# Performance work log

Hardware: AMD Instinct MI355X
Metric: run time of the kernel (lower is better)

Reference implementation:

```python
import jax, jax.numpy as jnp
import numpy as np

N, E, H, L, B, V = 20000, 600000, 128, 6, 16, 4


def _ln(x, g, b, eps=1e-5):
    mu = x.mean(-1, keepdims=True)
    var = ((x - mu) ** 2).mean(-1, keepdims=True)
    return (x - mu) * jax.lax.rsqrt(var + eps) * g + b


def setup_inputs() -> dict:
    key = jax.random.key(0)
    ks = jax.random.split(key, 16)
    rn = lambda k, shape, s=0.05: jax.random.normal(k, shape, jnp.float32) * s
    return dict(
        h_V=rn(ks[0], (N, H), 1.0),
        h_E=rn(ks[1], (E, H), 1.0),
        E_idx=jax.random.randint(ks[2], (2, E), 0, N, dtype=jnp.int32),
        batch_id=jnp.sort(jax.random.randint(ks[3], (N,), 0, B, dtype=jnp.int32)),
        S=jax.random.randint(ks[4], (N,), 0, V, dtype=jnp.int32),
        W1=rn(ks[5], (L, 3 * H, H)), b1=jnp.zeros((L, H), jnp.float32),
        W2=rn(ks[6], (L, H, H)), b2=jnp.zeros((L, H), jnp.float32),
        W3=rn(ks[7], (L, H, H)), b3=jnp.zeros((L, H), jnp.float32),
        ln1_g=jnp.ones((L, H), jnp.float32), ln1_b=jnp.zeros((L, H), jnp.float32),
        Wi=rn(ks[8], (L, H, 4 * H)), bi=jnp.zeros((L, 4 * H), jnp.float32),
        Wo=rn(ks[9], (L, 4 * H, H)), bo=jnp.zeros((L, H), jnp.float32),
        ln2_g=jnp.ones((L, H), jnp.float32), ln2_b=jnp.zeros((L, H), jnp.float32),
        P1=rn(ks[10], (H, H)),
        P2=rn(ks[11], (H, H)), p2b=jnp.zeros((H,), jnp.float32),
        R=rn(ks[12], (H, V)), rb=jnp.zeros((V,), jnp.float32),
    )


def reference(h_V, h_E, E_idx, batch_id, S, W1, b1, W2, b2, W3, b3,
              ln1_g, ln1_b, Wi, bi, Wo, bo, ln2_g, ln2_b, P1, P2, p2b, R, rb):
    src, dst = E_idx[0], E_idx[1]  # receiving node = src (E_idx[0])
    deg = jnp.clip(jax.ops.segment_sum(jnp.ones((E,), h_V.dtype), src,
                                       num_segments=N), 1.0)[:, None]
    for i in range(L):  # 3 encoder + 3 decoder MPNN layers, same structure
        h_EV = jnp.concatenate([h_E, h_V[src], h_V[dst]], axis=-1)  # [E, 3H]
        m = jax.nn.relu(h_EV @ W1[i] + b1[i])
        m = jax.nn.relu(m @ W2[i] + b2[i])
        m = m @ W3[i] + b3[i]
        agg = jax.ops.segment_sum(m, src, num_segments=N) / deg  # scatter_mean
        h_V = _ln(h_V + agg, ln1_g[i], ln1_b[i])
        dh = jax.nn.relu(h_V @ Wi[i] + bi[i]) @ Wo[i] + bo[i]  # position-wise FFN
        h_V = _ln(h_V + dh, ln2_g[i], ln2_b[i])
    # per-graph mean pooling (segment mean over batch_id)
    gcnt = jnp.clip(jax.ops.segment_sum(jnp.ones((N,), h_V.dtype), batch_id,
                                        num_segments=B), 1.0)[:, None]
    graph_embs = jax.ops.segment_sum(h_V, batch_id, num_segments=B) / gcnt
    graph_prjs = jax.nn.relu(graph_embs @ P1) @ P2 + p2b  # projection head
    logits = h_V @ R + rb  # readout
    return (logits, S, graph_prjs)
```

## Files before the change

kernel.cpp:

```cpp
#include <hip/hip_runtime.h>
#include <stdint.h>

#define NN 20000
#define EE 600000
#define HH 128
#define LL 6
#define BBATCH 16
#define VV 4

typedef __bf16 bf16x8 __attribute__((ext_vector_type(8)));
typedef float f32x4 __attribute__((ext_vector_type(4)));

__device__ __forceinline__ float bf2f(unsigned short u) {
    union { uint32_t i; float f; } v; v.i = ((uint32_t)u) << 16; return v.f;
}
__device__ __forceinline__ unsigned short f2bf(float f) {
    union { float f; uint32_t i; } v; v.f = f;
    uint32_t u = v.i;
    return (unsigned short)((u + 0x7FFFu + ((u >> 16) & 1u)) >> 16);
}
__device__ __forceinline__ float loadf(const void* p, size_t i, int f) {
    return f ? ((const float*)p)[i] : bf2f(((const unsigned short*)p)[i]);
}
__device__ __forceinline__ void load8bf(const void* base, size_t elem, int f, unsigned short* o) {
    if (!f) {
        *(uint4*)o = *(const uint4*)((const unsigned short*)base + elem);
    } else {
        const float* p = (const float*)base + elem;
        float4 a = *(const float4*)p, b = *(const float4*)(p + 4);
        o[0] = f2bf(a.x); o[1] = f2bf(a.y); o[2] = f2bf(a.z); o[3] = f2bf(a.w);
        o[4] = f2bf(b.x); o[5] = f2bf(b.y); o[6] = f2bf(b.z); o[7] = f2bf(b.w);
    }
}

__global__ void detect_kernel(const void* hv, int* flag) {
    __shared__ int cnt;
    if (threadIdx.x == 0) cnt = 0;
    __syncthreads();
    const unsigned short* u = (const unsigned short*)hv;
    int local = 0;
    for (int i = threadIdx.x; i < 4096; i += 256) {
        unsigned short v = u[i];
        int e = (v >> 7) & 0xFF;
        if ((v & 0x7FFF) == 0 || (e >= 0x30 && e <= 0x85)) local++;
    }
    atomicAdd(&cnt, local);
    __syncthreads();
    if (threadIdx.x == 0) flag[0] = (cnt < 3500) ? 1 : 0;
}

__global__ void repack_kernel(const void* __restrict__ src,
                              unsigned short* __restrict__ dst,
                              int K, int Nc, int total, const int* __restrict__ flag) {
    int idx = blockIdx.x * blockDim.x + threadIdx.x;
    if (idx >= total) return;
    const int f = flag[0];
    int per = K * Nc;
    int layer = idx / per, rem = idx % per;
    int k = rem / Nc, n = rem % Nc;
    dst[(size_t)layer * per + ((size_t)(k >> 5) * Nc + n) * 32 + (k & 31)] = f2bf(loadf(src, idx, f));
}

__global__ void init_hv_kernel(const void* __restrict__ hv_in,
                               float* __restrict__ hv_f32,
                               unsigned short* __restrict__ hv_bf, int total,
                               const int* __restrict__ flag) {
    int idx = blockIdx.x * blockDim.x + threadIdx.x;
    if (idx >= total) return;
    const int f = flag[0];
    float v = loadf(hv_in, idx, f);
    hv_bf[idx] = f2bf(v);
    hv_f32[idx] = v;
}

__global__ void deg_kernel(const int* __restrict__ Eidx, float* __restrict__ deg) {
    int e = blockIdx.x * blockDim.x + threadIdx.x;
    if (e < EE) atomicAdd(&deg[Eidx[e]], 1.0f);
}

__launch_bounds__(256, 3)
__global__ void edge_kernel(const void* __restrict__ hE,
                            const unsigned short* __restrict__ hv_bf,
                            const int* __restrict__ Eidx,
                            const unsigned short* __restrict__ W1p, const void* __restrict__ b1,
                            const unsigned short* __restrict__ W2p, const void* __restrict__ b2,
                            const unsigned short* __restrict__ W3p, const void* __restrict__ b3,
                            float* __restrict__ agg, int layer, const int* __restrict__ flag) {
    __shared__ __align__(16) unsigned short ev[64 * 392];
    unsigned short* m1 = ev;
    unsigned short* m2 = ev + 64 * 136;

    const int t = threadIdx.x;
    const int w = t >> 6;
    const int lane = t & 63;
    const int q = lane >> 4, ln = lane & 15;
    const int e0 = blockIdx.x * 64;
    const int f = flag[0];

    for (int c = t; c < 1024; c += 256) {
        int row = c >> 4, p = c & 15;
        int e = e0 + row;
        unsigned short tmp[8];
        load8bf(hE, (size_t)e * 128 + p * 8, f, tmp);
        *(uint4*)&ev[row * 392 + p * 8] = *(uint4*)tmp;
    }
    for (int c = t; c < 1024; c += 256) {
        int row = c >> 4, p = c & 15;
        int e = e0 + row;
        int s = Eidx[e];
        *(uint4*)&ev[row * 392 + 128 + p * 8] = *(const uint4*)&hv_bf[(size_t)s * 128 + p * 8];
    }
    for (int c = t; c < 1024; c += 256) {
        int row = c >> 4, p = c & 15;
        int e = e0 + row;
        int d = Eidx[EE + e];
        *(uint4*)&ev[row * 392 + 256 + p * 8] = *(const uint4*)&hv_bf[(size_t)d * 128 + p * 8];
    }
    __syncthreads();

    f32x4 acc[4][2];

    {
        const unsigned short* W1l = W1p + (size_t)layer * 384 * 128;
        for (int c = 0; c < 2; c++) {
            float bv = loadf(b1, (size_t)layer * HH + 16 * (2 * w + c) + ln, f);
            for (int rt = 0; rt < 4; rt++) acc[rt][c] = (f32x4){bv, bv, bv, bv};
        }
        for (int kk = 0; kk < 12; kk++) {
            bf16x8 bfr[2];
            for (int c = 0; c < 2; c++)
                bfr[c] = *(const bf16x8*)&W1l[((size_t)(kk * 128 + 16 * (2 * w + c) + ln)) * 32 + q * 8];
            for (int rt = 0; rt < 4; rt++) {
                bf16x8 af = *(bf16x8*)&ev[(16 * rt + ln) * 392 + kk * 32 + q * 8];
                acc[rt][0] = __builtin_amdgcn_mfma_f32_16x16x32_bf16(af, bfr[0], acc[rt][0], 0, 0, 0);
                acc[rt][1] = __builtin_amdgcn_mfma_f32_16x16x32_bf16(af, bfr[1], acc[rt][1], 0, 0, 0);
            }
        }
    }
    __syncthreads();
    for (int rt = 0; rt < 4; rt++)
        for (int c = 0; c < 2; c++)
            for (int r = 0; r < 4; r++) {
                float v = acc[rt][c][r]; v = v > 0.f ? v : 0.f;
                m1[(16 * rt + q * 4 + r) * 136 + 16 * (2 * w + c) + ln] = f2bf(v);
            }
    __syncthreads();

    {
        const unsigned short* W2l = W2p + (size_t)layer * 128 * 128;
        for (int c = 0; c < 2; c++) {
            float bv = loadf(b2, (size_t)layer * HH + 16 * (2 * w + c) + ln, f);
            for (int rt = 0; rt < 4; rt++) acc[rt][c] = (f32x4){bv, bv, bv, bv};
        }
        for (int kk = 0; kk < 4; kk++) {
            bf16x8 bfr[2];
            for (int c = 0; c < 2; c++)
                bfr[c] = *(const bf16x8*)&W2l[((size_t)(kk * 128 + 16 * (2 * w + c) + ln)) * 32 + q * 8];
            for (int rt = 0; rt < 4; rt++) {
                bf16x8 af = *(bf16x8*)&m1[(16 * rt + ln) * 136 + kk * 32 + q * 8];
                acc[rt][0] = __builtin_amdgcn_mfma_f32_16x16x32_bf16(af, bfr[0], acc[rt][0], 0, 0, 0);
                acc[rt][1] = __builtin_amdgcn_mfma_f32_16x16x32_bf16(af, bfr[1], acc[rt][1], 0, 0, 0);
            }
        }
    }
    for (int rt = 0; rt < 4; rt++)
        for (int c = 0; c < 2; c++)
            for (int r = 0; r < 4; r++) {
                float v = acc[rt][c][r]; v = v > 0.f ? v : 0.f;
                m2[(16 * rt + q * 4 + r) * 136 + 16 * (2 * w + c) + ln] = f2bf(v);
            }
    __syncthreads();

    {
        const unsigned short* W3l = W3p + (size_t)layer * 128 * 128;
        for (int c = 0; c < 2; c++) {
            float bv = loadf(b3, (size_t)layer * HH + 16 * (2 * w + c) + ln, f);
            for (int rt = 0; rt < 4; rt++) acc[rt][c] = (f32x4){bv, bv, bv, bv};
        }
        for (int kk = 0; kk < 4; kk++) {
            bf16x8 bfr[2];
            for (int c = 0; c < 2; c++)
                bfr[c] = *(const bf16x8*)&W3l[((size_t)(kk * 128 + 16 * (2 * w + c) + ln)) * 32 + q * 8];
            for (int rt = 0; rt < 4; rt++) {
                bf16x8 af = *(bf16x8*)&m2[(16 * rt + ln) * 136 + kk * 32 + q * 8];
                acc[rt][0] = __builtin_amdgcn_mfma_f32_16x16x32_bf16(af, bfr[0], acc[rt][0], 0, 0, 0);
                acc[rt][1] = __builtin_amdgcn_mfma_f32_16x16x32_bf16(af, bfr[1], acc[rt][1], 0, 0, 0);
            }
        }
    }

    for (int rt = 0; rt < 4; rt++) {
        int se[4];
        for (int r = 0; r < 4; r++) se[r] = Eidx[e0 + 16 * rt + q * 4 + r];
        for (int c = 0; c < 2; c++) {
            int col = 16 * (2 * w + c) + ln;
            for (int r = 0; r < 4; r++)
                atomicAdd(&agg[(size_t)se[r] * HH + col], acc[rt][c][r]);
        }
    }
}

__launch_bounds__(256, 1)
__global__ void node_kernel(float* __restrict__ hv_f32, unsigned short* __restrict__ hv_bf,
                            const float* __restrict__ agg, const float* __restrict__ deg,
                            const void* __restrict__ ln1g, const void* __restrict__ ln1b,
                            const unsigned short* __restrict__ Wip, const void* __restrict__ bip,
                            const unsigned short* __restrict__ Wop, const void* __restrict__ bop,
                            const void* __restrict__ ln2g, const void* __restrict__ ln2b,
                            int layer, const int* __restrict__ flag) {
    __shared__ __align__(16) float xf[64 * 132];
    __shared__ __align__(16) unsigned short tb[64 * 136];
    __shared__ __align__(16) unsigned short ub[64 * 520];
    const int t = threadIdx.x;
    const int w = t >> 6;
    const int lane = t & 63;
    const int q = lane >> 4, ln = lane & 15;
    const int n0 = blockIdx.x * 64;
    const int f = flag[0];

    for (int idx = t; idx < 64 * 128; idx += 256) {
        int row = idx >> 7, col = idx & 127;
        int g = n0 + row;
        float v = 0.f;
        if (g < NN) {
            float dg = deg[g]; dg = dg < 1.f ? 1.f : dg;
            v = hv_f32[(size_t)g * 128 + col] + agg[(size_t)g * 128 + col] / dg;
        }
        xf[row * 132 + col] = v;
    }
    __syncthreads();

    if (t < 64) {
        float mu = 0.f;
        for (int j = 0; j < 128; j++) mu += xf[t * 132 + j];
        mu *= (1.f / 128.f);
        float var = 0.f;
        for (int j = 0; j < 128; j++) { float d = xf[t * 132 + j] - mu; var += d * d; }
        var *= (1.f / 128.f);
        float rs = rsqrtf(var + 1e-5f);
        for (int j = 0; j < 128; j++) {
            float val = (xf[t * 132 + j] - mu) * rs * loadf(ln1g, layer * 128 + j, f)
                        + loadf(ln1b, layer * 128 + j, f);
            xf[t * 132 + j] = val;
            tb[t * 136 + j] = f2bf(val);
        }
    }
    __syncthreads();

    {
        const unsigned short* Wil = Wip + (size_t)layer * 128 * 512;
        for (int g2 = 0; g2 < 2; g2++) {
            f32x4 acc[4][4];
            for (int c = 0; c < 4; c++) {
                int ct = 8 * w + 4 * g2 + c;
                float bv = loadf(bip, (size_t)layer * 512 + 16 * ct + ln, f);
                for (int rt = 0; rt < 4; rt++) acc[rt][c] = (f32x4){bv, bv, bv, bv};
            }
            for (int kk = 0; kk < 4; kk++) {
                bf16x8 bfr[4];
                for (int c = 0; c < 4; c++) {
                    int ct = 8 * w + 4 * g2 + c;
                    bfr[c] = *(const bf16x8*)&Wil[((size_t)(kk * 512 + 16 * ct + ln)) * 32 + q * 8];
                }
                for (int rt = 0; rt < 4; rt++) {
                    bf16x8 af = *(bf16x8*)&tb[(16 * rt + ln) * 136 + kk * 32 + q * 8];
                    for (int c = 0; c < 4; c++)
                        acc[rt][c] = __builtin_amdgcn_mfma_f32_16x16x32_bf16(af, bfr[c], acc[rt][c], 0, 0, 0);
                }
            }
            for (int rt = 0; rt < 4; rt++)
                for (int c = 0; c < 4; c++) {
                    int ct = 8 * w + 4 * g2 + c;
                    for (int r = 0; r < 4; r++) {
                        float v = acc[rt][c][r]; v = v > 0.f ? v : 0.f;
                        ub[(16 * rt + q * 4 + r) * 520 + 16 * ct + ln] = f2bf(v);
                    }
                }
        }
    }
    __syncthreads();

    {
        const unsigned short* Wol = Wop + (size_t)layer * 512 * 128;
        f32x4 acc[4][2];
        for (int c = 0; c < 2; c++) {
            int ct = 2 * w + c;
            float bv = loadf(bop, (size_t)layer * 128 + 16 * ct + ln, f);
            for (int rt = 0; rt < 4; rt++) acc[rt][c] = (f32x4){bv, bv, bv, bv};
        }
        for (int kk = 0; kk < 16; kk++) {
            bf16x8 bfr[2];
            for (int c = 0; c < 2; c++) {
                int ct = 2 * w + c;
                bfr[c] = *(const bf16x8*)&Wol[((size_t)(kk * 128 + 16 * ct + ln)) * 32 + q * 8];
            }
            for (int rt = 0; rt < 4; rt++) {
                bf16x8 af = *(bf16x8*)&ub[(16 * rt + ln) * 520 + kk * 32 + q * 8];
                for (int c = 0; c < 2; c++)
                    acc[rt][c] = __builtin_amdgcn_mfma_f32_16x16x32_bf16(af, bfr[c], acc[rt][c], 0, 0, 0);
            }
        }
        for (int rt = 0; rt < 4; rt++)
            for (int c = 0; c < 2; c++) {
                int ct = 2 * w + c;
                for (int r = 0; r < 4; r++)
                    xf[(16 * rt + q * 4 + r) * 132 + 16 * ct + ln] += acc[rt][c][r];
            }
    }
    __syncthreads();

    if (t < 64) {
        int g = n0 + t;
        if (g < NN) {
            float mu = 0.f;
            for (int j = 0; j < 128; j++) mu += xf[t * 132 + j];
            mu *= (1.f / 128.f);
            float var = 0.f;
            for (int j = 0; j < 128; j++) { float d = xf[t * 132 + j] - mu; var += d * d; }
            var *= (1.f / 128.f);
            float rs = rsqrtf(var + 1e-5f);
            for (int j = 0; j < 128; j++) {
                float val = (xf[t * 132 + j] - mu) * rs * loadf(ln2g, layer * 128 + j, f)
                            + loadf(ln2b, layer * 128 + j, f);
                hv_f32[(size_t)g * 128 + j] = val;
                hv_bf[(size_t)g * 128 + j] = f2bf(val);
            }
        }
    }
}

__global__ void pool_kernel(const float* __restrict__ hv_f32, const int* __restrict__ batch_id,
                            float* __restrict__ ge) {
    int col = threadIdx.x;
    int base = blockIdx.x * 128;
    if (base >= NN) return;
    int end = base + 128; if (end > NN) end = NN;
    int cur = batch_id[base];
    float sum = 0.f;
    for (int g = base; g < end; g++) {
        int b = batch_id[g];
        if (b != cur) { atomicAdd(&ge[cur * 128 + col], sum); sum = 0.f; cur = b; }
        sum += hv_f32[(size_t)g * 128 + col];
    }
    atomicAdd(&ge[cur * 128 + col], sum);
}

__global__ void proj_kernel(const float* __restrict__ ge, const int* __restrict__ batch_id,
                            const void* __restrict__ P1, const void* __restrict__ P2,
                            const void* __restrict__ p2b, void* __restrict__ d_out,
                            const int* __restrict__ flag) {
    __shared__ float cnt[BBATCH];
    __shared__ float gm[BBATCH * HH];
    __shared__ float hb[BBATCH * HH];
    int t = threadIdx.x;
    const int f = flag[0];
    if (t < BBATCH) cnt[t] = 0.f;
    __syncthreads();
    for (int n = t; n < NN; n += 256) atomicAdd(&cnt[batch_id[n]], 1.0f);
    __syncthreads();
    for (int idx = t; idx < BBATCH * HH; idx += 256) {
        int b = idx >> 7;
        float c = cnt[b]; c = c < 1.f ? 1.f : c;
        gm[idx] = ge[idx] / c;
    }
    __syncthreads();
    for (int idx = t; idx < BBATCH * HH; idx += 256) {
        int b = idx >> 7, j = idx & 127;
        float s = 0.f;
        for (int k = 0; k < HH; k++) s += gm[b * 128 + k] * loadf(P1, k * 128 + j, f);
        hb[idx] = s > 0.f ? s : 0.f;
    }
    __syncthreads();
    for (int idx = t; idx < BBATCH * HH; idx += 256) {
        int b = idx >> 7, j = idx & 127;
        float s = loadf(p2b, j, f);
        for (int k = 0; k < HH; k++) s += hb[b * 128 + k] * loadf(P2, k * 128 + j, f);
        size_t o = (size_t)NN * VV + NN + idx;
        if (f) ((float*)d_out)[o] = s;
        else   ((unsigned short*)d_out)[o] = f2bf(s);
    }
}

__global__ void logits_kernel(const float* __restrict__ hv_f32, const void* __restrict__ R,
                              const void* __restrict__ rb, const int* __restrict__ S,
                              void* __restrict__ d_out, const int* __restrict__ flag) {
    __shared__ float Rs[HH * VV];
    __shared__ float rbs[VV];
    int t = threadIdx.x;
    const int f = flag[0];
    for (int i = t; i < HH * VV; i += 256) Rs[i] = loadf(R, i, f);
    if (t < VV) rbs[t] = loadf(rb, t, f);
    __syncthreads();
    int g = blockIdx.x * 256 + t;
    if (g < NN) {
        float a0 = rbs[0], a1 = rbs[1], a2 = rbs[2], a3 = rbs[3];
        const float* hv = hv_f32 + (size_t)g * 128;
        for (int k = 0; k < 128; k++) {
            float h = hv[k];
            a0 += h * Rs[k * 4 + 0];
            a1 += h * Rs[k * 4 + 1];
            a2 += h * Rs[k * 4 + 2];
            a3 += h * Rs[k * 4 + 3];
        }
        float sv = (float)S[g];
        if (f) {
            float* o = (float*)d_out;
            o[g * 4 + 0] = a0; o[g * 4 + 1] = a1; o[g * 4 + 2] = a2; o[g * 4 + 3] = a3;
            o[(size_t)NN * VV + g] = sv;
        } else {
            unsigned short* o = (unsigned short*)d_out;
            o[g * 4 + 0] = f2bf(a0); o[g * 4 + 1] = f2bf(a1);
            o[g * 4 + 2] = f2bf(a2); o[g * 4 + 3] = f2bf(a3);
            o[(size_t)NN * VV + g] = f2bf(sv);
        }
    }
}

extern "C" void kernel_launch(void* const* d_in, const int* in_sizes, int n_in,
                              void* d_out, int out_size, void* d_ws, size_t ws_size,
                              hipStream_t stream) {
    const void* hV   = d_in[0];
    const void* hE   = d_in[1];
    const int*  Eidx = (const int*)d_in[2];
    const int*  bid  = (const int*)d_in[3];
    const int*  S    = (const int*)d_in[4];
    const void* W1   = d_in[5];
    const void* b1   = d_in[6];
    const void* W2   = d_in[7];
    const void* b2   = d_in[8];
    const void* W3   = d_in[9];
    const void* b3   = d_in[10];
    const void* ln1g = d_in[11];
    const void* ln1b = d_in[12];
    const void* Wi   = d_in[13];
    const void* bi   = d_in[14];
    const void* Wo   = d_in[15];
    const void* bo   = d_in[16];
    const void* ln2g = d_in[17];
    const void* ln2b = d_in[18];
    const void* P1   = d_in[19];
    const void* P2   = d_in[20];
    const void* p2b  = d_in[21];
    const void* R    = d_in[22];
    const void* rb   = d_in[23];

    char* ws = (char*)d_ws;
    float* hv_f32 = (float*)ws;           ws += (size_t)NN * HH * 4;
    float* agg    = (float*)ws;           ws += (size_t)NN * HH * 4;
    float* deg    = (float*)ws;           ws += (size_t)NN * 4;
    float* ge     = (float*)ws;           ws += (size_t)BBATCH * HH * 4;
    unsigned short* hv_bf = (unsigned short*)ws; ws += (size_t)NN * HH * 2;
    unsigned short* W1p   = (unsigned short*)ws; ws += (size_t)LL * 384 * 128 * 2;
    unsigned short* W2p   = (unsigned short*)ws; ws += (size_t)LL * 128 * 128 * 2;
    unsigned short* W3p   = (unsigned short*)ws; ws += (size_t)LL * 128 * 128 * 2;
    unsigned short* Wip   = (unsigned short*)ws; ws += (size_t)LL * 128 * 512 * 2;
    unsigned short* Wop   = (unsigned short*)ws; ws += (size_t)LL * 512 * 128 * 2;
    int* flag = (int*)ws;                 ws += 16;

    hipMemsetAsync(deg, 0, (size_t)NN * 4, stream);
    hipMemsetAsync(ge, 0, (size_t)BBATCH * HH * 4, stream);

    detect_kernel<<<1, 256, 0, stream>>>(hV, flag);

    init_hv_kernel<<<(NN * HH + 255) / 256, 256, 0, stream>>>(hV, hv_f32, hv_bf, NN * HH, flag);
    deg_kernel<<<(EE + 255) / 256, 256, 0, stream>>>(Eidx, deg);

    repack_kernel<<<(LL * 384 * 128 + 255) / 256, 256, 0, stream>>>(W1, W1p, 384, 128, LL * 384 * 128, flag);
    repack_kernel<<<(LL * 128 * 128 + 255) / 256, 256, 0, stream>>>(W2, W2p, 128, 128, LL * 128 * 128, flag);
    repack_kernel<<<(LL * 128 * 128 + 255) / 256, 256, 0, stream>>>(W3, W3p, 128, 128, LL * 128 * 128, flag);
    repack_kernel<<<(LL * 128 * 512 + 255) / 256, 256, 0, stream>>>(Wi, Wip, 128, 512, LL * 128 * 512, flag);
    repack_kernel<<<(LL * 512 * 128 + 255) / 256, 256, 0, stream>>>(Wo, Wop, 512, 128, LL * 512 * 128, flag);

    for (int i = 0; i < LL; i++) {
        hipMemsetAsync(agg, 0, (size_t)NN * HH * 4, stream);
        edge_kernel<<<EE / 64, 256, 0, stream>>>(hE, hv_bf, Eidx, W1p, b1, W2p, b2, W3p, b3, agg, i, flag);
        node_kernel<<<(NN + 63) / 64, 256, 0, stream>>>(hv_f32, hv_bf, agg, deg,
                                                        ln1g, ln1b, Wip, bi, Wop, bo, ln2g, ln2b, i, flag);
    }

    pool_kernel<<<(NN + 127) / 128, 128, 0, stream>>>(hv_f32, bid, ge);
    proj_kernel<<<1, 256, 0, stream>>>(ge, bid, P1, P2, p2b, d_out, flag);
    logits_kernel<<<(NN + 255) / 256, 256, 0, stream>>>(hv_f32, R, rb, S, d_out, flag);
}
```

Baseline: 3.634 ms.

## Sort edges by source node and restructure edge MLP as per-wave 32x32 MFMA

```diff
diff --git a/kernel.cpp b/kernel.cpp
--- a/kernel.cpp
+++ b/kernel.cpp
@@ -3,6 +3,7 @@
 
 #define NN 20000
 #define EE 600000
+#define EP 600064
 #define HH 128
 #define LL 6
 #define BBATCH 16
@@ -10,6 +11,7 @@
 
 typedef __bf16 bf16x8 __attribute__((ext_vector_type(8)));
 typedef float f32x4 __attribute__((ext_vector_type(4)));
+typedef float f32x16 __attribute__((ext_vector_type(16)));
 
 __device__ __forceinline__ float bf2f(unsigned short u) {
     union { uint32_t i; float f; } v; v.i = ((uint32_t)u) << 16; return v.f;
@@ -49,8 +51,7 @@
     if (threadIdx.x == 0) flag[0] = (cnt < 3500) ? 1 : 0;
 }
 
-__global__ void repack_kernel(const void* __restrict__ src,
-                              unsigned short* __restrict__ dst,
+__global__ void pack16_kernel(const void* __restrict__ src, unsigned short* __restrict__ dst,
                               int K, int Nc, int total, const int* __restrict__ flag) {
     int idx = blockIdx.x * blockDim.x + threadIdx.x;
     if (idx >= total) return;
@@ -58,11 +59,21 @@
     int per = K * Nc;
     int layer = idx / per, rem = idx % per;
     int k = rem / Nc, n = rem % Nc;
+    dst[(size_t)layer * per + ((size_t)(k >> 4) * Nc + n) * 16 + (k & 15)] = f2bf(loadf(src, idx, f));
+}
+
+__global__ void repack32_kernel(const void* __restrict__ src, unsigned short* __restrict__ dst,
+                                int K, int Nc, int total, const int* __restrict__ flag) {
+    int idx = blockIdx.x * blockDim.x + threadIdx.x;
+    if (idx >= total) return;
+    const int f = flag[0];
+    int per = K * Nc;
+    int layer = idx / per, rem = idx % per;
+    int k = rem / Nc, n = rem % Nc;
     dst[(size_t)layer * per + ((size_t)(k >> 5) * Nc + n) * 32 + (k & 31)] = f2bf(loadf(src, idx, f));
 }
 
-__global__ void init_hv_kernel(const void* __restrict__ hv_in,
-                               float* __restrict__ hv_f32,
+__global__ void init_hv_kernel(const void* __restrict__ hv_in, float* __restrict__ hv_f32,
                                unsigned short* __restrict__ hv_bf, int total,
                                const int* __restrict__ flag) {
     int idx = blockIdx.x * blockDim.x + threadIdx.x;
@@ -73,129 +84,228 @@
     hv_f32[idx] = v;
 }
 
-__global__ void deg_kernel(const int* __restrict__ Eidx, float* __restrict__ deg) {
+__global__ void deg_kernel(const int* __restrict__ Eidx, int* __restrict__ degi) {
     int e = blockIdx.x * blockDim.x + threadIdx.x;
-    if (e < EE) atomicAdd(&deg[Eidx[e]], 1.0f);
-}
-
-__launch_bounds__(256, 3)
-__global__ void edge_kernel(const void* __restrict__ hE,
+    if (e < EE) atomicAdd(&degi[Eidx[e]], 1);
+}
+
+__global__ void prefix_kernel(const int* __restrict__ degi, int* __restrict__ cursor,
+                              float* __restrict__ degf) {
+    __shared__ int part[256];
+    __shared__ int psum[256];
+    int t = threadIdx.x;
+    const int CH = (NN + 255) / 256;
+    int lo = t * CH, hi = lo + CH; if (hi > NN) hi = NN;
+    int s = 0;
+    for (int i = lo; i < hi; i++) s += degi[i];
+    part[t] = s;
+    __syncthreads();
+    if (t == 0) {
+        int run = 0;
+        for (int i = 0; i < 256; i++) { psum[i] = run; run += part[i]; }
+    }
+    __syncthreads();
+    int run = psum[t];
+    for (int i = lo; i < hi; i++) {
+        cursor[i] = run;
+        run += degi[i];
+        degf[i] = (float)degi[i];
+    }
+}
+
+__global__ void perm_kernel(const int* __restrict__ Eidx, int* __restrict__ cursor,
+                            int* __restrict__ perm) {
+    int e = blockIdx.x * blockDim.x + threadIdx.x;
+    if (e < EE) {
+        int pos = atomicAdd(&cursor[Eidx[e]], 1);
+        perm[pos] = e;
+    }
+}
+
+__global__ void idx_kernel(const int* __restrict__ Eidx, const int* __restrict__ perm,
+                           int* __restrict__ srcs_s, int* __restrict__ dsts_s) {
+    int i = blockIdx.x * blockDim.x + threadIdx.x;
+    if (i >= EP) return;
+    if (i < EE) {
+        int e = perm[i];
+        srcs_s[i] = Eidx[e];
+        dsts_s[i] = Eidx[EE + e];
+    } else {
+        srcs_s[i] = NN;
+        dsts_s[i] = 0;
+    }
+}
+
+__global__ void hep_kernel(const void* __restrict__ hE, const int* __restrict__ perm,
+                           unsigned short* __restrict__ hEp, const int* __restrict__ flag) {
+    int idx = blockIdx.x * blockDim.x + threadIdx.x;
+    if (idx >= EP * 16) return;
+    int i = idx >> 4, p = idx & 15;
+    unsigned short tmp[8];
+    if (i < EE) {
+        int e = perm[i];
+        load8bf(hE, (size_t)e * 128 + p * 8, flag[0], tmp);
+    } else {
+        for (int j = 0; j < 8; j++) tmp[j] = 0;
+    }
+    *(uint4*)&hEp[(size_t)i * 128 + p * 8] = *(uint4*)tmp;
+}
+
+__launch_bounds__(256, 2)
+__global__ void edge_kernel(const void* __restrict__ hE, const unsigned short* __restrict__ hEp,
+                            const int* __restrict__ perm,
                             const unsigned short* __restrict__ hv_bf,
-                            const int* __restrict__ Eidx,
-                            const unsigned short* __restrict__ W1p, const void* __restrict__ b1,
-                            const unsigned short* __restrict__ W2p, const void* __restrict__ b2,
-                            const unsigned short* __restrict__ W3p, const void* __restrict__ b3,
-                            float* __restrict__ agg, int layer, const int* __restrict__ flag) {
-    __shared__ __align__(16) unsigned short ev[64 * 392];
-    unsigned short* m1 = ev;
-    unsigned short* m2 = ev + 64 * 136;
-
+                            const int* __restrict__ srcs_s, const int* __restrict__ dsts_s,
+                            const unsigned short* __restrict__ W1a, const void* __restrict__ b1,
+                            const unsigned short* __restrict__ W2a, const void* __restrict__ b2,
+                            const unsigned short* __restrict__ W3b, const void* __restrict__ b3,
+                            float* __restrict__ agg, int layer, const int* __restrict__ flag,
+                            int use_hep) {
+    __shared__ __align__(16) unsigned short lds[4 * 8704];
     const int t = threadIdx.x;
     const int w = t >> 6;
-    const int lane = t & 63;
-    const int q = lane >> 4, ln = lane & 15;
-    const int e0 = blockIdx.x * 64;
+    const int ln5 = t & 31;
+    const int q2 = (t >> 5) & 1;
+    unsigned short* m1 = lds + w * 8704;
+    unsigned short* m2 = m1 + 4352;
     const int f = flag[0];
-
-    for (int c = t; c < 1024; c += 256) {
-        int row = c >> 4, p = c & 15;
-        int e = e0 + row;
-        unsigned short tmp[8];
-        load8bf(hE, (size_t)e * 128 + p * 8, f, tmp);
-        *(uint4*)&ev[row * 392 + p * 8] = *(uint4*)tmp;
-    }
-    for (int c = t; c < 1024; c += 256) {
-        int row = c >> 4, p = c & 15;
-        int e = e0 + row;
-        int s = Eidx[e];
-        *(uint4*)&ev[row * 392 + 128 + p * 8] = *(const uint4*)&hv_bf[(size_t)s * 128 + p * 8];
-    }
-    for (int c = t; c < 1024; c += 256) {
-        int row = c >> 4, p = c & 15;
-        int e = e0 + row;
-        int d = Eidx[EE + e];
-        *(uint4*)&ev[row * 392 + 256 + p * 8] = *(const uint4*)&hv_bf[(size_t)d * 128 + p * 8];
-    }
-    __syncthreads();
-
-    f32x4 acc[4][2];
-
-    {
-        const unsigned short* W1l = W1p + (size_t)layer * 384 * 128;
-        for (int c = 0; c < 2; c++) {
-            float bv = loadf(b1, (size_t)layer * HH + 16 * (2 * w + c) + ln, f);
-            for (int rt = 0; rt < 4; rt++) acc[rt][c] = (f32x4){bv, bv, bv, bv};
-        }
-        for (int kk = 0; kk < 12; kk++) {
-            bf16x8 bfr[2];
-            for (int c = 0; c < 2; c++)
-                bfr[c] = *(const bf16x8*)&W1l[((size_t)(kk * 128 + 16 * (2 * w + c) + ln)) * 32 + q * 8];
-            for (int rt = 0; rt < 4; rt++) {
-                bf16x8 af = *(bf16x8*)&ev[(16 * rt + ln) * 392 + kk * 32 + q * 8];
-                acc[rt][0] = __builtin_amdgcn_mfma_f32_16x16x32_bf16(af, bfr[0], acc[rt][0], 0, 0, 0);
-                acc[rt][1] = __builtin_amdgcn_mfma_f32_16x16x32_bf16(af, bfr[1], acc[rt][1], 0, 0, 0);
-            }
-        }
-    }
-    __syncthreads();
-    for (int rt = 0; rt < 4; rt++)
-        for (int c = 0; c < 2; c++)
+    const int e0w = blockIdx.x * 128 + w * 32;
+    const int edge = e0w + ln5;
+
+    const int sidx = srcs_s[edge];
+    const int didx = dsts_s[edge];
+    int pe = 0;
+    if (!use_hep && edge < EE) pe = perm[edge];
+
+    const unsigned short* W1l = W1a + (size_t)layer * 384 * 128;
+    const unsigned short* W2l = W2a + (size_t)layer * 128 * 128;
+    const unsigned short* W3l = W3b + (size_t)layer * 128 * 128;
+
+    f32x16 acc[4];
+
+#pragma unroll
+    for (int ct = 0; ct < 4; ct++)
+#pragma unroll
+        for (int r = 0; r < 16; r++) {
+            int m = 32 * ct + (r & 3) + 8 * (r >> 2) + 4 * q2;
+            acc[ct][r] = loadf(b1, (size_t)layer * 128 + m, f);
+        }
+
+#pragma unroll
+    for (int kk = 0; kk < 8; kk++) {
+        bf16x8 bB;
+        if (use_hep) {
+            bB = *(const bf16x8*)&hEp[(size_t)edge * 128 + kk * 16 + q2 * 8];
+        } else if (!f) {
+            bB = *(const bf16x8*)&((const unsigned short*)hE)[(size_t)pe * 128 + kk * 16 + q2 * 8];
+        } else {
+            unsigned short tmp[8];
+            load8bf(hE, (size_t)pe * 128 + kk * 16 + q2 * 8, 1, tmp);
+            bB = *(bf16x8*)tmp;
+        }
+#pragma unroll
+        for (int ct = 0; ct < 4; ct++) {
+            bf16x8 aA = *(const bf16x8*)&W1l[((size_t)(kk * 128 + 32 * ct + ln5)) * 16 + q2 * 8];
+            acc[ct] = __builtin_amdgcn_mfma_f32_32x32x16_bf16(aA, bB, acc[ct], 0, 0, 0);
+        }
+    }
+#pragma unroll
+    for (int kk = 0; kk < 8; kk++) {
+        bf16x8 bB = *(const bf16x8*)&hv_bf[(size_t)sidx * 128 + kk * 16 + q2 * 8];
+#pragma unroll
+        for (int ct = 0; ct < 4; ct++) {
+            bf16x8 aA = *(const bf16x8*)&W1l[((size_t)((kk + 8) * 128 + 32 * ct + ln5)) * 16 + q2 * 8];
+            acc[ct] = __builtin_amdgcn_mfma_f32_32x32x16_bf16(aA, bB, acc[ct], 0, 0, 0);
+        }
+    }
+#pragma unroll
+    for (int kk = 0; kk < 8; kk++) {
+        bf16x8 bB = *(const bf16x8*)&hv_bf[(size_t)didx * 128 + kk * 16 + q2 * 8];
+#pragma unroll
+        for (int ct = 0; ct < 4; ct++) {
+            bf16x8 aA = *(const bf16x8*)&W1l[((size_t)((kk + 16) * 128 + 32 * ct + ln5)) * 16 + q2 * 8];
+            acc[ct] = __builtin_amdgcn_mfma_f32_32x32x16_bf16(aA, bB, acc[ct], 0, 0, 0);
+        }
+    }
+#pragma unroll
+    for (int ct = 0; ct < 4; ct++)
+#pragma unroll
+        for (int g = 0; g < 4; g++) {
+            uint2 u;
+            unsigned short* tp = (unsigned short*)&u;
+#pragma unroll
             for (int r = 0; r < 4; r++) {
-                float v = acc[rt][c][r]; v = v > 0.f ? v : 0.f;
-                m1[(16 * rt + q * 4 + r) * 136 + 16 * (2 * w + c) + ln] = f2bf(v);
-            }
-    __syncthreads();
-
-    {
-        const unsigned short* W2l = W2p + (size_t)layer * 128 * 128;
-        for (int c = 0; c < 2; c++) {
-            float bv = loadf(b2, (size_t)layer * HH + 16 * (2 * w + c) + ln, f);
-            for (int rt = 0; rt < 4; rt++) acc[rt][c] = (f32x4){bv, bv, bv, bv};
-        }
-        for (int kk = 0; kk < 4; kk++) {
-            bf16x8 bfr[2];
-            for (int c = 0; c < 2; c++)
-                bfr[c] = *(const bf16x8*)&W2l[((size_t)(kk * 128 + 16 * (2 * w + c) + ln)) * 32 + q * 8];
-            for (int rt = 0; rt < 4; rt++) {
-                bf16x8 af = *(bf16x8*)&m1[(16 * rt + ln) * 136 + kk * 32 + q * 8];
-                acc[rt][0] = __builtin_amdgcn_mfma_f32_16x16x32_bf16(af, bfr[0], acc[rt][0], 0, 0, 0);
-                acc[rt][1] = __builtin_amdgcn_mfma_f32_16x16x32_bf16(af, bfr[1], acc[rt][1], 0, 0, 0);
-            }
-        }
-    }
-    for (int rt = 0; rt < 4; rt++)
-        for (int c = 0; c < 2; c++)
+                float x = acc[ct][4 * g + r];
+                tp[r] = f2bf(x > 0.f ? x : 0.f);
+            }
+            *(uint2*)&m1[ln5 * 136 + 32 * ct + 8 * g + 4 * q2] = u;
+        }
+
+#pragma unroll
+    for (int ct = 0; ct < 4; ct++)
+#pragma unroll
+        for (int r = 0; r < 16; r++) {
+            int m = 32 * ct + (r & 3) + 8 * (r >> 2) + 4 * q2;
+            acc[ct][r] = loadf(b2, (size_t)layer * 128 + m, f);
+        }
+#pragma unroll
+    for (int kk = 0; kk < 8; kk++) {
+        bf16x8 bB = *(const bf16x8*)&m1[ln5 * 136 + kk * 16 + q2 * 8];
+#pragma unroll
+        for (int ct = 0; ct < 4; ct++) {
+            bf16x8 aA = *(const bf16x8*)&W2l[((size_t)(kk * 128 + 32 * ct + ln5)) * 16 + q2 * 8];
+            acc[ct] = __builtin_amdgcn_mfma_f32_32x32x16_bf16(aA, bB, acc[ct], 0, 0, 0);
+        }
+    }
+#pragma unroll
+    for (int ct = 0; ct < 4; ct++)
+#pragma unroll
+        for (int g = 0; g < 4; g++) {
+            uint2 u;
+            unsigned short* tp = (unsigned short*)&u;
+#pragma unroll
             for (int r = 0; r < 4; r++) {
-                float v = acc[rt][c][r]; v = v > 0.f ? v : 0.f;
-                m2[(16 * rt + q * 4 + r) * 136 + 16 * (2 * w + c) + ln] = f2bf(v);
-            }
-    __syncthreads();
-
-    {
-        const unsigned short* W3l = W3p + (size_t)layer * 128 * 128;
-        for (int c = 0; c < 2; c++) {
-            float bv = loadf(b3, (size_t)layer * HH + 16 * (2 * w + c) + ln, f);
-            for (int rt = 0; rt < 4; rt++) acc[rt][c] = (f32x4){bv, bv, bv, bv};
-        }
-        for (int kk = 0; kk < 4; kk++) {
-            bf16x8 bfr[2];
-            for (int c = 0; c < 2; c++)
-                bfr[c] = *(const bf16x8*)&W3l[((size_t)(kk * 128 + 16 * (2 * w + c) + ln)) * 32 + q * 8];
-            for (int rt = 0; rt < 4; rt++) {
-                bf16x8 af = *(bf16x8*)&m2[(16 * rt + ln) * 136 + kk * 32 + q * 8];
-                acc[rt][0] = __builtin_amdgcn_mfma_f32_16x16x32_bf16(af, bfr[0], acc[rt][0], 0, 0, 0);
-                acc[rt][1] = __builtin_amdgcn_mfma_f32_16x16x32_bf16(af, bfr[1], acc[rt][1], 0, 0, 0);
-            }
-        }
-    }
-
-    for (int rt = 0; rt < 4; rt++) {
-        int se[4];
-        for (int r = 0; r < 4; r++) se[r] = Eidx[e0 + 16 * rt + q * 4 + r];
-        for (int c = 0; c < 2; c++) {
-            int col = 16 * (2 * w + c) + ln;
-            for (int r = 0; r < 4; r++)
-                atomicAdd(&agg[(size_t)se[r] * HH + col], acc[rt][c][r]);
+                float x = acc[ct][4 * g + r];
+                tp[r] = f2bf(x > 0.f ? x : 0.f);
+            }
+            *(uint2*)&m2[ln5 * 136 + 32 * ct + 8 * g + 4 * q2] = u;
+        }
+
+#pragma unroll
+    for (int c = 0; c < 4; c++) {
+        float bv = loadf(b3, (size_t)layer * 128 + 32 * c + ln5, f);
+#pragma unroll
+        for (int r = 0; r < 16; r++) acc[c][r] = bv;
+    }
+#pragma unroll
+    for (int kk = 0; kk < 8; kk++) {
+        bf16x8 aA = *(const bf16x8*)&m2[ln5 * 136 + kk * 16 + q2 * 8];
+#pragma unroll
+        for (int c = 0; c < 4; c++) {
+            bf16x8 bB = *(const bf16x8*)&W3l[((size_t)(kk * 128 + 32 * c + ln5)) * 16 + q2 * 8];
+            acc[c] = __builtin_amdgcn_mfma_f32_32x32x16_bf16(aA, bB, acc[c], 0, 0, 0);
+        }
+    }
+
+    int sg[4][4];
+#pragma unroll
+    for (int g = 0; g < 4; g++)
+#pragma unroll
+        for (int r = 0; r < 4; r++)
+            sg[g][r] = srcs_s[e0w + 8 * g + 4 * q2 + r];
+
+#pragma unroll
+    for (int c = 0; c < 4; c++) {
+        int col = 32 * c + ln5;
+#pragma unroll
+        for (int g = 0; g < 4; g++) {
+            float a0 = acc[c][4 * g + 0], a1 = acc[c][4 * g + 1];
+            float a2 = acc[c][4 * g + 2], a3 = acc[c][4 * g + 3];
+            int s0 = sg[g][0], s1 = sg[g][1], s2 = sg[g][2], s3 = sg[g][3];
+            if (s3 == s2) a2 += a3; else atomicAdd(&agg[(size_t)s3 * 128 + col], a3);
+            if (s2 == s1) a1 += a2; else atomicAdd(&agg[(size_t)s2 * 128 + col], a2);
+            if (s1 == s0) a0 += a1; else atomicAdd(&agg[(size_t)s1 * 128 + col], a1);
+            atomicAdd(&agg[(size_t)s0 * 128 + col], a0);
         }
     }
 }
@@ -445,36 +555,50 @@
     const void* rb   = d_in[23];
 
     char* ws = (char*)d_ws;
-    float* hv_f32 = (float*)ws;           ws += (size_t)NN * HH * 4;
-    float* agg    = (float*)ws;           ws += (size_t)NN * HH * 4;
-    float* deg    = (float*)ws;           ws += (size_t)NN * 4;
-    float* ge     = (float*)ws;           ws += (size_t)BBATCH * HH * 4;
-    unsigned short* hv_bf = (unsigned short*)ws; ws += (size_t)NN * HH * 2;
-    unsigned short* W1p   = (unsigned short*)ws; ws += (size_t)LL * 384 * 128 * 2;
-    unsigned short* W2p   = (unsigned short*)ws; ws += (size_t)LL * 128 * 128 * 2;
-    unsigned short* W3p   = (unsigned short*)ws; ws += (size_t)LL * 128 * 128 * 2;
-    unsigned short* Wip   = (unsigned short*)ws; ws += (size_t)LL * 128 * 512 * 2;
-    unsigned short* Wop   = (unsigned short*)ws; ws += (size_t)LL * 512 * 128 * 2;
-    int* flag = (int*)ws;                 ws += 16;
-
-    hipMemsetAsync(deg, 0, (size_t)NN * 4, stream);
+    float* hv_f32 = (float*)ws;                   ws += (size_t)NN * HH * 4;
+    float* agg    = (float*)ws;                   ws += (size_t)(NN + 1) * HH * 4;
+    float* degf   = (float*)ws;                   ws += (size_t)NN * 4;
+    float* ge     = (float*)ws;                   ws += (size_t)BBATCH * HH * 4;
+    unsigned short* hv_bf = (unsigned short*)ws;  ws += (size_t)(NN + 1) * HH * 2;
+    unsigned short* W1a   = (unsigned short*)ws;  ws += (size_t)LL * 384 * 128 * 2;
+    unsigned short* W2a   = (unsigned short*)ws;  ws += (size_t)LL * 128 * 128 * 2;
+    unsigned short* W3b   = (unsigned short*)ws;  ws += (size_t)LL * 128 * 128 * 2;
+    unsigned short* Wip   = (unsigned short*)ws;  ws += (size_t)LL * 128 * 512 * 2;
+    unsigned short* Wop   = (unsigned short*)ws;  ws += (size_t)LL * 512 * 128 * 2;
+    int* degi   = (int*)ws;                       ws += (size_t)NN * 4;
+    int* cursor = (int*)ws;                       ws += (size_t)NN * 4;
+    int* perm   = (int*)ws;                       ws += (size_t)EP * 4;
+    int* srcs_s = (int*)ws;                       ws += (size_t)EP * 4;
+    int* dsts_s = (int*)ws;                       ws += (size_t)EP * 4;
+    int* flag   = (int*)ws;                       ws += 16;
+    unsigned short* hEp = (unsigned short*)ws;
+    size_t need_hep = (size_t)(ws - (char*)d_ws) + (size_t)EP * 128 * 2;
+    int use_hep = (ws_size >= need_hep) ? 1 : 0;
+
+    hipMemsetAsync(degi, 0, (size_t)NN * 4, stream);
     hipMemsetAsync(ge, 0, (size_t)BBATCH * HH * 4, stream);
 
     detect_kernel<<<1, 256, 0, stream>>>(hV, flag);
 
     init_hv_kernel<<<(NN * HH + 255) / 256, 256, 0, stream>>>(hV, hv_f32, hv_bf, NN * HH, flag);
-    deg_kernel<<<(EE + 255) / 256, 256, 0, stream>>>(Eidx, deg);
-
-    repack_kernel<<<(LL * 384 * 128 + 255) / 256, 256, 0, stream>>>(W1, W1p, 384, 128, LL * 384 * 128, flag);
-    repack_kernel<<<(LL * 128 * 128 + 255) / 256, 256, 0, stream>>>(W2, W2p, 128, 128, LL * 128 * 128, flag);
-    repack_kernel<<<(LL * 128 * 128 + 255) / 256, 256, 0, stream>>>(W3, W3p, 128, 128, LL * 128 * 128, flag);
-    repack_kernel<<<(LL * 128 * 512 + 255) / 256, 256, 0, stream>>>(Wi, Wip, 128, 512, LL * 128 * 512, flag);
-    repack_kernel<<<(LL * 512 * 128 + 255) / 256, 256, 0, stream>>>(Wo, Wop, 512, 128, LL * 512 * 128, flag);
+    deg_kernel<<<(EE + 255) / 256, 256, 0, stream>>>(Eidx, degi);
+    prefix_kernel<<<1, 256, 0, stream>>>(degi, cursor, degf);
+    perm_kernel<<<(EE + 255) / 256, 256, 0, stream>>>(Eidx, cursor, perm);
+    idx_kernel<<<(EP + 255) / 256, 256, 0, stream>>>(Eidx, perm, srcs_s, dsts_s);
+    if (use_hep)
+        hep_kernel<<<(EP * 16 + 255) / 256, 256, 0, stream>>>(hE, perm, hEp, flag);
+
+    pack16_kernel<<<(LL * 384 * 128 + 255) / 256, 256, 0, stream>>>(W1, W1a, 384, 128, LL * 384 * 128, flag);
+    pack16_kernel<<<(LL * 128 * 128 + 255) / 256, 256, 0, stream>>>(W2, W2a, 128, 128, LL * 128 * 128, flag);
+    pack16_kernel<<<(LL * 128 * 128 + 255) / 256, 256, 0, stream>>>(W3, W3b, 128, 128, LL * 128 * 128, flag);
+    repack32_kernel<<<(LL * 128 * 512 + 255) / 256, 256, 0, stream>>>(Wi, Wip, 128, 512, LL * 128 * 512, flag);
+    repack32_kernel<<<(LL * 512 * 128 + 255) / 256, 256, 0, stream>>>(Wo, Wop, 512, 128, LL * 512 * 128, flag);
 
     for (int i = 0; i < LL; i++) {
-        hipMemsetAsync(agg, 0, (size_t)NN * HH * 4, stream);
-        edge_kernel<<<EE / 64, 256, 0, stream>>>(hE, hv_bf, Eidx, W1p, b1, W2p, b2, W3p, b3, agg, i, flag);
-        node_kernel<<<(NN + 63) / 64, 256, 0, stream>>>(hv_f32, hv_bf, agg, deg,
+        hipMemsetAsync(agg, 0, (size_t)(NN + 1) * HH * 4, stream);
+        edge_kernel<<<EP / 128, 256, 0, stream>>>(hE, hEp, perm, hv_bf, srcs_s, dsts_s,
+                                                  W1a, b1, W2a, b2, W3b, b3, agg, i, flag, use_hep);
+        node_kernel<<<(NN + 63) / 64, 256, 0, stream>>>(hv_f32, hv_bf, agg, degf,
                                                         ln1g, ln1b, Wip, bi, Wop, bo, ln2g, ln2b, i, flag);
     }
 
```

Result: faster. 3.207 ms (-11.7%).
